# Performance work log

Hardware: AMD Instinct MI355X
Metric: run time of the kernel (lower is better)

## Reference

```python
import jax, jax.numpy as jnp
import numpy as np

B, L = 16, 512          # samples x tokens-per-sample
S = B * L               # total packed tokens
H, HKV, D = 16, 4, 128  # query heads, kv heads, head_dim
G = H // HKV            # GQA group size
HID = 2048
EPS = 1e-6


def rmsnorm(x, w):
    # Qwen2RMSNorm: fp32 variance, scale by weight
    v = jnp.mean(x.astype(jnp.float32) ** 2, axis=-1, keepdims=True)
    return (x.astype(jnp.float32) * jax.lax.rsqrt(v + EPS)).astype(x.dtype) * w


def rotate_half(x):
    x1, x2 = jnp.split(x, 2, axis=-1)
    return jnp.concatenate([-x2, x1], axis=-1)


def setup_inputs() -> dict:
    key = jax.random.key(0)
    ks = jax.random.split(key, 24)
    f = lambda k, shp, s=0.02: (jax.random.normal(k, shp, dtype=jnp.float32) * s)
    inp = {
        'packed_sequence_und': f(ks[0], (S // 2, HID), 1.0),
        'packed_sequence_gen': f(ks[1], (S // 2, HID), 1.0),
        # und tokens on even slots, gen on odd slots -> irregular scatter
        'packed_und_token_indexes': jnp.arange(0, S, 2, dtype=jnp.int32),
        'packed_gen_token_indexes': jnp.arange(1, S, 2, dtype=jnp.int32),
        # und-path projections (q/k/v have bias, o does not)
        'q_w': f(ks[2], (H * D, HID)), 'q_b': f(ks[3], (H * D,)),
        'k_w': f(ks[4], (HKV * D, HID)), 'k_b': f(ks[5], (HKV * D,)),
        'v_w': f(ks[6], (HKV * D, HID)), 'v_b': f(ks[7], (HKV * D,)),
        'o_w': f(ks[8], (HID, H * D)),
        # gen-path (moe_gen) projections
        'q_w_g': f(ks[9], (H * D, HID)), 'q_b_g': f(ks[10], (H * D,)),
        'k_w_g': f(ks[11], (HKV * D, HID)), 'k_b_g': f(ks[12], (HKV * D,)),
        'v_w_g': f(ks[13], (HKV * D, HID)), 'v_b_g': f(ks[14], (HKV * D,)),
        'o_w_g': f(ks[15], (HID, H * D)),
        # qk-norm weights
        'qn_w': jnp.ones((D,), jnp.float32), 'kn_w': jnp.ones((D,), jnp.float32),
        'qn_w_g': jnp.ones((D,), jnp.float32), 'kn_w_g': jnp.ones((D,), jnp.float32),
    }
    # RoPE cos/sin for packed positions (position resets per sample)
    pos = jnp.tile(jnp.arange(L, dtype=jnp.float32), B)            # [S]
    inv_freq = 1.0 / (1e6 ** (jnp.arange(0, D, 2, dtype=jnp.float32) / D))
    freqs = pos[:, None] * inv_freq[None, :]                       # [S, D/2]
    emb = jnp.concatenate([freqs, freqs], axis=-1)                 # [S, D]
    inp['packed_cos'] = jnp.cos(emb)
    inp['packed_sin'] = jnp.sin(emb)
    return inp


def reference(packed_sequence_und, packed_sequence_gen, packed_cos, packed_sin,
              packed_und_token_indexes, packed_gen_token_indexes,
              q_w, q_b, k_w, k_b, v_w, v_b, o_w,
              q_w_g, q_b_g, k_w_g, k_b_g, v_w_g, v_b_g, o_w_g,
              qn_w, kn_w, qn_w_g, kn_w_g):
    ui, gi = packed_und_token_indexes, packed_gen_token_indexes
    # dual-path QKV projection + index scatter into shared packed buffers
    q = jnp.zeros((S, H * D), jnp.float32)
    q = q.at[ui].set(packed_sequence_und @ q_w.T + q_b)
    q = q.at[gi].set(packed_sequence_gen @ q_w_g.T + q_b_g)
    k = jnp.zeros((S, HKV * D), jnp.float32)
    k = k.at[ui].set(packed_sequence_und @ k_w.T + k_b)
    k = k.at[gi].set(packed_sequence_gen @ k_w_g.T + k_b_g)
    v = jnp.zeros((S, HKV * D), jnp.float32)
    v = v.at[ui].set(packed_sequence_und @ v_w.T + v_b)
    v = v.at[gi].set(packed_sequence_gen @ v_w_g.T + v_b_g)

    q = q.reshape(S, H, D)
    k = k.reshape(S, HKV, D)
    v = v.reshape(S, HKV, D)

    # per-stream QK RMSNorm, scattered back
    q = jnp.zeros_like(q).at[ui].set(rmsnorm(q[ui], qn_w)).at[gi].set(rmsnorm(q[gi], qn_w_g))
    k = jnp.zeros_like(k).at[ui].set(rmsnorm(k[ui], kn_w)).at[gi].set(rmsnorm(k[gi], kn_w_g))

    # RoPE (unsqueeze_dim=1)
    cos, sin = packed_cos[:, None, :], packed_sin[:, None, :]
    q = q * cos + rotate_half(q) * sin
    k = k * cos + rotate_half(k) * sin

    # block-diagonal causal attention over packed samples (GQA)
    qb_ = q.reshape(B, L, HKV, G, D)
    kb_ = k.reshape(B, L, HKV, D)
    vb_ = v.reshape(B, L, HKV, D)
    scale = 1.0 / np.sqrt(D)
    scores = jnp.einsum('bqhgd,bkhd->bhgqk', qb_, kb_) * scale   # [B,HKV,G,L,L]
    causal = jnp.tril(jnp.ones((L, L), bool))
    scores = jnp.where(causal, scores, -jnp.inf)
    probs = jax.nn.softmax(scores, axis=-1)
    out = jnp.einsum('bhgqk,bkhd->bqhgd', probs, vb_)            # [B,L,HKV,G,D]
    out = out.reshape(S, H * D)

    out_und = out[ui] @ o_w.T
    out_gen = out[gi] @ o_w_g.T
    return (out_und, out_gen)
```

## Files before the change

### kernel.cpp

```cpp
#include <hip/hip_runtime.h>

typedef __bf16 bf16;
typedef __bf16 bf16x8 __attribute__((ext_vector_type(8)));
typedef float  f32x4  __attribute__((ext_vector_type(4)));

#define HALF   4096
#define S_TOT  8192
#define HID    2048
#define NH     16
#define NKV    4
#define DH     128
#define LSEQ   512

typedef const __attribute__((address_space(1))) void* as1_cvp;
typedef __attribute__((address_space(3))) void* as3_vp;

__device__ __forceinline__ void gl2lds16(const void* g, void* l) {
    __builtin_amdgcn_global_load_lds((as1_cvp)g, (as3_vp)l, 16, 0, 0);
}

#define VMCNT(n) asm volatile("s_waitcnt vmcnt(" #n ")" ::: "memory")

struct CvtArgs {
    const float* src[10];
    bf16*        dst[10];
    int          n4[10];
};
__global__ __launch_bounds__(256) void k_convert_multi(CvtArgs a, int total4) {
    int i = blockIdx.x * 256 + threadIdx.x;
    if (i >= total4) return;
    int off = i;
    #pragma unroll
    for (int s = 0; s < 10; ++s) {
        if (off < a.n4[s]) {
            float4 v = ((const float4*)a.src[s])[off];
            union { bf16 b[4]; ushort4 u; } t;
            t.b[0] = (bf16)v.x; t.b[1] = (bf16)v.y; t.b[2] = (bf16)v.z; t.b[3] = (bf16)v.w;
            ((ushort4*)a.dst[s])[off] = t.u;
            return;
        }
        off -= a.n4[s];
    }
}

__global__ void k_invtyp(const int* __restrict__ ui, const int* __restrict__ gi,
                         int* __restrict__ it) {
    int t = blockIdx.x * 256 + threadIdx.x;
    if (t < HALF) { it[ui[t]] = t << 1; it[gi[t]] = (t << 1) | 1; }
}

#define C0 0
#define C1 16384
#define C2 32768
#define C3 49152

#define STG2(MB, KC, DST)                                                       \
    gl2lds16((MB) + (KC) + go0, (DST) + wave*1024);                             \
    gl2lds16((MB) + (KC) + go1, (DST) + 8192 + wave*1024);

#define PH(RD, MH, DOB, STG, TAIL)                                              \
  {                                                                             \
    _Pragma("unroll")                                                           \
    for (int im = 0; im < 4; ++im)                                              \
        a_[im] = *(const bf16x8*)(sAb + (RD) + (MH)*4096 + im*1024 + abase);    \
    if (DOB) {                                                                  \
        _Pragma("unroll")                                                       \
        for (int jn = 0; jn < 4; ++jn)                                          \
            b_[jn] = *(const bf16x8*)(sBb + (RD) + jn*1024 + bbase);            \
    }                                                                           \
    STG;                                                                        \
    __builtin_amdgcn_s_barrier();                                               \
    __builtin_amdgcn_s_setprio(1);                                              \
    _Pragma("unroll")                                                           \
    for (int im = 0; im < 4; ++im)                                              \
      _Pragma("unroll")                                                         \
      for (int jn = 0; jn < 4; ++jn)                                            \
        acc[(MH)*4+im][jn] = __builtin_amdgcn_mfma_f32_16x16x32_bf16(           \
            a_[im], b_[jn], acc[(MH)*4+im][jn], 0, 0, 0);                       \
    __builtin_amdgcn_s_setprio(0);                                              \
    TAIL;                                                                       \
    __builtin_amdgcn_s_barrier();                                               \
  }

__device__ __forceinline__ void gemm256_core(
    const bf16* __restrict__ A, const bf16* __restrict__ B,
    int m0, int n0, int tid, char* sAb, char* sBb, f32x4 (&acc)[8][4])
{
    const int lane = tid & 63;
    const int lm = lane & 15, kq = lane >> 4;
    const int wave = tid >> 6;
    const int wm = wave >> 2, wn = wave & 3;

    const int swz16 = (kq ^ ((lm >> 1) & 3)) * 16;
    const int abase = wm*8192 + lm*64 + swz16;
    const int bbase = wn*4096 + lm*64 + swz16;

    int go0, go1;
    {
        const int s0 = tid,        r0 = s0 >> 2, c0 = (s0 & 3) ^ ((r0 >> 1) & 3);
        const int s1 = 512 + tid,  r1 = s1 >> 2, c1 = (s1 & 3) ^ ((r1 >> 1) & 3);
        go0 = r0*HID + c0*8;
        go1 = r1*HID + c1*8;
    }
    const bf16* Ab = A + (size_t)m0*HID;
    const bf16* Bb = B + (size_t)n0*HID;

    bf16x8 a_[4], b_[4];

    STG2(Ab, 0,  sAb + C0);  STG2(Ab, 32, sAb + C1);
    STG2(Bb, 0,  sBb + C0);  STG2(Bb, 32, sBb + C1);
    STG2(Ab, 64, sAb + C2);  STG2(Bb, 64, sBb + C2);
    VMCNT(4);
    __builtin_amdgcn_s_barrier();

    #pragma unroll 1
    for (int i = 0; i < 15; ++i) {
        const int kc = 128*i;
        PH(C0, 0, 1, STG2(Ab, kc+96,  sAb+C3), (void)0);
        PH(C0, 1, 0, STG2(Bb, kc+96,  sBb+C3), (void)0);
        PH(C1, 0, 1, STG2(Ab, kc+128, sAb+C0), (void)0);
        PH(C1, 1, 0, STG2(Bb, kc+128, sBb+C0), VMCNT(4));
        PH(C2, 0, 1, STG2(Ab, kc+160, sAb+C1), (void)0);
        PH(C2, 1, 0, STG2(Bb, kc+160, sBb+C1), (void)0);
        PH(C3, 0, 1, STG2(Ab, kc+192, sAb+C2), (void)0);
        PH(C3, 1, 0, STG2(Bb, kc+192, sBb+C2), VMCNT(4));
    }
    {
        PH(C0, 0, 1, STG2(Ab, 2016, sAb+C3), (void)0);
        PH(C0, 1, 0, STG2(Bb, 2016, sBb+C3), (void)0);
        PH(C1, 0, 1, (void)0, (void)0);
        PH(C1, 1, 0, (void)0, VMCNT(0));
        PH(C2, 0, 1, (void)0, (void)0);
        PH(C2, 1, 0, (void)0, (void)0);
        PH(C3, 0, 1, (void)0, (void)0);
        PH(C3, 1, 0, (void)0, (void)0);
    }
}

__global__ __launch_bounds__(512, 2) void k_gemm_qkv(
    const bf16* __restrict__ Xu, const bf16* __restrict__ Xg,
    const bf16* __restrict__ Wu, const bf16* __restrict__ Wg,
    const float* __restrict__ qbu, const float* __restrict__ kbu, const float* __restrict__ vbu,
    const float* __restrict__ qbg, const float* __restrict__ kbg, const float* __restrict__ vbg,
    const int* __restrict__ ui, const int* __restrict__ gi,
    bf16* __restrict__ qo, bf16* __restrict__ ko, bf16* __restrict__ vo)
{
    __shared__ __align__(16) bf16 sA[4][256*32];
    __shared__ __align__(16) bf16 sB[4][256*32];

    const int lin = blockIdx.x;
    const int idx = (lin & 7) * 48 + (lin >> 3);
    const int gen = idx / 192;
    const int rem = idx - gen * 192;
    const int my  = rem / 12;
    const int nx_ = rem - my * 12;
    const int m0 = my * 256, n0 = nx_ * 256;

    const bf16* X = gen ? Xg : Xu;
    const bf16* W = gen ? Wg : Wu;
    const float* qb = gen ? qbg : qbu;
    const float* kb = gen ? kbg : kbu;
    const float* vb = gen ? vbg : vbu;
    const int* idxmap = gen ? gi : ui;

    const int tid = threadIdx.x;
    const int wave = tid >> 6, lane = tid & 63;
    const int lm = lane & 15, kq = lane >> 4;
    const int wm = wave >> 2, wn = wave & 3;

    f32x4 acc[8][4] = {};
    gemm256_core(X, W, m0, n0, tid, (char*)&sA[0][0], (char*)&sB[0][0], acc);

    #pragma unroll
    for (int im = 0; im < 8; ++im) {
        int srow[4];
        #pragma unroll
        for (int r = 0; r < 4; ++r) srow[r] = idxmap[m0 + wm*128 + im*16 + kq*4 + r];
        #pragma unroll
        for (int jn = 0; jn < 4; ++jn) {
            const int o = n0 + wn*64 + jn*16 + lm;
            bf16* dst; float bias; int off0, ld;
            if (o < 2048)      { dst = qo; ld = 2048; off0 = o;        bias = qb[o]; }
            else if (o < 2560) { dst = ko; ld = 512;  off0 = o - 2048; bias = kb[o-2048]; }
            else               { dst = vo; ld = 512;  off0 = o - 2560; bias = vb[o-2560]; }
            #pragma unroll
            for (int r = 0; r < 4; ++r)
                dst[(size_t)srow[r]*ld + off0] = (bf16)(acc[im][jn][r] + bias);
        }
    }
}

__global__ __launch_bounds__(256) void k_norm_rope(
    bf16* __restrict__ qbuf, bf16* __restrict__ kbuf,
    const float* __restrict__ cosb, const float* __restrict__ sinb,
    const int* __restrict__ invtyp,
    const float* __restrict__ qnu, const float* __restrict__ qng,
    const float* __restrict__ knu, const float* __restrict__ kng)
{
    const int row = blockIdx.x * 4 + (threadIdx.x >> 6);
    const int lane = threadIdx.x & 63;
    const int s = row / (NH + NKV), hh = row % (NH + NKV);
    const int isg = invtyp[s] & 1;
    bf16* ptr; const float* w; float qs;
    if (hh < NH) { ptr = qbuf + (size_t)s*HID + hh*DH;           w = isg ? qng : qnu;
                   qs = 0.08838834764831845f * 1.4426950408889634f; }
    else         { ptr = kbuf + (size_t)s*(NKV*DH) + (hh-NH)*DH; w = isg ? kng : knu;
                   qs = 1.0f; }

    const unsigned u = *(const unsigned*)((const unsigned short*)ptr + 2*lane);
    const float f0 = __uint_as_float(u << 16);
    const float f1 = __uint_as_float(u & 0xffff0000u);
    float ss = f0*f0 + f1*f1;
    #pragma unroll
    for (int m = 32; m; m >>= 1) ss += __shfl_xor(ss, m, 64);
    const float r = rsqrtf(ss * (1.0f/128.0f) + 1e-6f);
    const float2 wv = *(const float2*)(w + 2*lane);
    const float xn0 = f0 * r * wv.x;
    const float xn1 = f1 * r * wv.y;
    const float po0 = __shfl_xor(xn0, 32, 64);
    const float po1 = __shfl_xor(xn1, 32, 64);
    const float2 c2 = *(const float2*)(cosb + (size_t)s*DH + 2*lane);
    const float2 s2 = *(const float2*)(sinb + (size_t)s*DH + 2*lane);
    const float sg = (lane < 32) ? -1.0f : 1.0f;
    const float o0 = (xn0 * c2.x + sg * po0 * s2.x) * qs;
    const float o1 = (xn1 * c2.y + sg * po1 * s2.y) * qs;
    union { unsigned short us[2]; unsigned u; } t;
    bf16 b0 = (bf16)o0, b1 = (bf16)o1;
    t.us[0] = *(unsigned short*)&b0; t.us[1] = *(unsigned short*)&b1;
    *(unsigned*)((unsigned short*)ptr + 2*lane) = t.u;
}

__global__ __launch_bounds__(256) void k_vtrans(const bf16* __restrict__ v, bf16* __restrict__ vt)
{
    __shared__ __align__(16) bf16 sT[64 * 132];
    const int kvh = blockIdx.y;
    const int s0 = blockIdx.x * 64;
    const int b = s0 >> 9;
    const int pos0 = s0 & 511;
    const int tid = threadIdx.x;

    #pragma unroll
    for (int i = 0; i < 4; ++i) {
        const int c = i*256 + tid;
        const int rowi = c >> 4, col8 = c & 15;
        const uint4 d = *(const uint4*)(v + (size_t)(s0 + rowi)*(NKV*DH) + kvh*DH + col8*8);
        uint2* lp = (uint2*)&sT[rowi*132 + col8*8];
        lp[0] = make_uint2(d.x, d.y);
        lp[1] = make_uint2(d.z, d.w);
    }
    __syncthreads();
    const int dd = tid >> 1, half = tid & 1;
    __align__(16) bf16 tmp[32];
    #pragma unroll
    for (int p = 0; p < 32; ++p) tmp[p] = sT[(half*32 + p)*132 + dd];
    bf16* dst = vt + ((size_t)(b*NKV + kvh)*DH + dd)*LSEQ + pos0 + half*32;
    #pragma unroll
    for (int q = 0; q < 8; ++q) ((ushort4*)dst)[q] = ((ushort4*)tmp)[q];
}

__global__ __launch_bounds__(256) void k_attn(
    const bf16* __restrict__ qbuf, const bf16* __restrict__ kbuf,
    const bf16* __restrict__ vt, const int* __restrict__ invtyp,
    bf16* __restrict__ aop_u, bf16* __restrict__ aop_g)
{
    __shared__ __align__(16) bf16 sK[2][64*128];
    __shared__ __align__(16) bf16 sV[2][128*64];
    __shared__ __align__(16) bf16 sP[4][16*72];

    const int qt = 7 - blockIdx.x;
    const int h = blockIdx.y, b = blockIdx.z;
    const int kvh = h >> 2;
    const int tid = threadIdx.x, wave = tid >> 6, lane = tid & 63;
    const int lm = lane & 15, kq = lane >> 4;
    const int q0 = qt * 64;

    bf16x8 qfrag[4];
    {
        const bf16* qp = qbuf + ((size_t)(b*LSEQ + q0 + wave*16 + lm))*HID + h*DH;
        #pragma unroll
        for (int ks = 0; ks < 4; ++ks)
            qfrag[ks] = *(const bf16x8*)(qp + ks*32 + kq*8);
    }

    const bf16* kbase = kbuf + ((size_t)(b*LSEQ))*(NKV*DH) + kvh*DH;
    const bf16* vbase = vt + ((size_t)(b*NKV + kvh)*DH)*LSEQ;

    f32x4 accO[8] = {};
    float lpart[4] = {0.f, 0.f, 0.f, 0.f};
    bf16* const sPw = &sP[wave][0];

    {
        const bf16* kp = kbase;
        const bf16* vp = vbase;
        #pragma unroll
        for (int i = 0; i < 4; ++i) {
            const int g = i*4 + wave;
            const int ch = g*64 + lane;
            { const int row = ch >> 4, cp = ch & 15;
              const int c = (cp & 8) | ((cp ^ row) & 7);
              gl2lds16(kp + (size_t)row*(NKV*DH) + c*8, (char*)&sK[0][0] + (size_t)g*1024); }
            { const int d = ch >> 3, cp = ch & 7;
              const int c = (cp ^ d) & 7;
              gl2lds16(vp + (size_t)d*LSEQ + c*8, (char*)&sV[0][0] + (size_t)g*1024); }
        }
    }

    for (int kt = 0; kt <= qt; ++kt) {
        const int cur = kt & 1;
        __syncthreads();

        if (kt < qt) {
            const bf16* kp = kbase + (size_t)((kt+1)*64)*(NKV*DH);
            const bf16* vp = vbase + (kt+1)*64;
            const int nxt = cur ^ 1;
            #pragma unroll
            for (int i = 0; i < 4; ++i) {
                const int g = i*4 + wave;
                const int ch = g*64 + lane;
                { const int row = ch >> 4, cp = ch & 15;
                  const int c = (cp & 8) | ((cp ^ row) & 7);
                  gl2lds16(kp + (size_t)row*(NKV*DH) + c*8, (char*)&sK[nxt][0] + (size_t)g*1024); }
                { const int d = ch >> 3, cp = ch & 7;
                  const int c = (cp ^ d) & 7;
                  gl2lds16(vp + (size_t)d*LSEQ + c*8, (char*)&sV[nxt][0] + (size_t)g*1024); }
            }
        }

        f32x4 s4[4] = {};
        #pragma unroll
        for (int ks = 0; ks < 4; ++ks) {
            const int cq = ks*4 + kq;
            const int cs = (cq & 8) | ((cq ^ lm) & 7);
            #pragma unroll
            for (int nt = 0; nt < 4; ++nt) {
                bf16x8 bk = *(const bf16x8*)&sK[cur][(nt*16 + lm)*128 + cs*8];
                s4[nt] = __builtin_amdgcn_mfma_f32_16x16x32_bf16(qfrag[ks], bk, s4[nt], 0, 0, 0);
            }
        }

        const bool diag = (kt == qt);
        #pragma unroll
        for (int r = 0; r < 4; ++r) {
            const int rloc = wave*16 + kq*4 + r;
            float v0 = s4[0][r], v1 = s4[1][r], v2 = s4[2][r], v3 = s4[3][r];
            if (diag) {
                if (lm      > rloc) v0 = -1e30f;
                if (lm + 16 > rloc) v1 = -1e30f;
                if (lm + 32 > rloc) v2 = -1e30f;
                if (lm + 48 > rloc) v3 = -1e30f;
            }
            const float p0 = exp2f(v0);
            const float p1 = exp2f(v1);
            const float p2 = exp2f(v2);
            const float p3 = exp2f(v3);
            lpart[r] += (p0 + p1) + (p2 + p3);
            const int prow = (kq*4 + r) * 72;
            sPw[prow + lm]      = (bf16)p0;
            sPw[prow + 16 + lm] = (bf16)p1;
            sPw[prow + 32 + lm] = (bf16)p2;
            sPw[prow + 48 + lm] = (bf16)p3;
        }

        #pragma unroll
        for (int pc = 0; pc < 2; ++pc) {
            bf16x8 ap = *(const bf16x8*)&sPw[lm*72 + pc*32 + kq*8];
            #pragma unroll
            for (int dt = 0; dt < 8; ++dt) {
                const int cv = (pc*4 + kq);
                const int cs = (cv ^ lm) & 7;
                bf16x8 bv = *(const bf16x8*)&sV[cur][(dt*16 + lm)*64 + cs*8];
                accO[dt] = __builtin_amdgcn_mfma_f32_16x16x32_bf16(ap, bv, accO[dt], 0, 0, 0);
            }
        }
    }

    #pragma unroll
    for (int r = 0; r < 4; ++r) {
        float l = lpart[r];
        l += __shfl_xor(l, 1, 64);
        l += __shfl_xor(l, 2, 64);
        l += __shfl_xor(l, 4, 64);
        l += __shfl_xor(l, 8, 64);
        const int srow = b*LSEQ + q0 + wave*16 + kq*4 + r;
        const int code = invtyp[srow];
        bf16* dst = (code & 1) ? aop_g : aop_u;
        const size_t off = (size_t)(code >> 1)*HID + h*DH;
        const float inv_l = 1.0f / l;
        #pragma unroll
        for (int dt = 0; dt < 8; ++dt)
            dst[off + dt*16 + lm] = (bf16)(accO[dt][r] * inv_l);
    }
}

__global__ __launch_bounds__(512, 2) void k_gemm_out(
    const bf16* __restrict__ Au, const bf16* __restrict__ Ag,
    const bf16* __restrict__ Wu, const bf16* __restrict__ Wg,
    float* __restrict__ out)
{
    __shared__ __align__(16) bf16 sA[4][256*32];
    __shared__ __align__(16) bf16 sB[4][256*32];

    const int lin = blockIdx.x;
    const int idx = (lin & 7) * 32 + (lin >> 3);
    const int gen = idx / 128;
    const int rem = idx - gen * 128;
    const int my  = rem >> 3;
    const int nx_ = rem & 7;
    const int m0 = my * 256, n0 = nx_ * 256;

    const bf16* A = gen ? Ag : Au;
    const bf16* W = gen ? Wg : Wu;
    float* O = out + (size_t)gen * HALF * HID;

    const int tid = threadIdx.x;
    const int wave = tid >> 6, lane = tid & 63;
    const int lm = lane & 15, kq = lane >> 4;
    const int wm = wave >> 2, wn = wave & 3;

    f32x4 acc[8][4] = {};
    gemm256_core(A, W, m0, n0, tid, (char*)&sA[0][0], (char*)&sB[0][0], acc);

    #pragma unroll
    for (int im = 0; im < 8; ++im)
        #pragma unroll
        for (int jn = 0; jn < 4; ++jn)
            #pragma unroll
            for (int r = 0; r < 4; ++r)
                O[(size_t)(m0 + wm*128 + im*16 + kq*4 + r)*HID + (n0 + wn*64 + jn*16 + lm)]
                    = acc[im][jn][r];
}

extern "C" void kernel_launch(void* const* d_in, const int* in_sizes, int n_in,
                              void* d_out, int out_size, void* d_ws, size_t ws_size,
                              hipStream_t stream)
{
    (void)in_sizes; (void)n_in; (void)out_size; (void)ws_size;
    const float* x_u  = (const float*)d_in[0];
    const float* x_g  = (const float*)d_in[1];
    const int*   ui   = (const int*)d_in[2];
    const int*   gi   = (const int*)d_in[3];
    const float* q_w  = (const float*)d_in[4];
    const float* q_b  = (const float*)d_in[5];
    const float* k_w  = (const float*)d_in[6];
    const float* k_b  = (const float*)d_in[7];
    const float* v_w  = (const float*)d_in[8];
    const float* v_b  = (const float*)d_in[9];
    const float* o_w  = (const float*)d_in[10];
    const float* q_wg = (const float*)d_in[11];
    const float* q_bg = (const float*)d_in[12];
    const float* k_wg = (const float*)d_in[13];
    const float* k_bg = (const float*)d_in[14];
    const float* v_wg = (const float*)d_in[15];
    const float* v_bg = (const float*)d_in[16];
    const float* o_wg = (const float*)d_in[17];
    const float* qn_u = (const float*)d_in[18];
    const float* kn_u = (const float*)d_in[19];
    const float* qn_g = (const float*)d_in[20];
    const float* kn_g = (const float*)d_in[21];
    const float* cosb = (const float*)d_in[22];
    const float* sinb = (const float*)d_in[23];

    char* w = (char*)d_ws;
    auto alloc = [&](size_t bytes) { char* p = w; w += (bytes + 255) & ~(size_t)255; return p; };
    bf16* xb_u   = (bf16*)alloc((size_t)HALF*HID*2);
    bf16* xb_g   = (bf16*)alloc((size_t)HALF*HID*2);
    bf16* wqkv_u = (bf16*)alloc((size_t)3072*HID*2);
    bf16* wqkv_g = (bf16*)alloc((size_t)3072*HID*2);
    bf16* wo_u   = (bf16*)alloc((size_t)HID*HID*2);
    bf16* wo_g   = (bf16*)alloc((size_t)HID*HID*2);
    bf16* qbuf   = (bf16*)alloc((size_t)S_TOT*HID*2);
    bf16* kbuf   = (bf16*)alloc((size_t)S_TOT*NKV*DH*2);
    bf16* vbuf   = (bf16*)alloc((size_t)S_TOT*NKV*DH*2);
    bf16* vtb    = (bf16*)alloc((size_t)S_TOT*NKV*DH*2);
    int*  invtyp = (int*)alloc((size_t)S_TOT*4);
    bf16* aop_u = xb_u;
    bf16* aop_g = xb_g;

    CvtArgs ca;
    int total4 = 0, si = 0;
    auto seg = [&](const float* s, bf16* d, size_t n) {
        ca.src[si] = s; ca.dst[si] = d; ca.n4[si] = (int)(n / 4);
        total4 += (int)(n / 4); ++si;
    };
    seg(x_u,  xb_u,                (size_t)HALF*HID);
    seg(x_g,  xb_g,                (size_t)HALF*HID);
    seg(q_w,  wqkv_u,              (size_t)2048*HID);
    seg(k_w,  wqkv_u + 2048*HID,   (size_t)512*HID);
    seg(v_w,  wqkv_u + 2560*HID,   (size_t)512*HID);
    seg(q_wg, wqkv_g,              (size_t)2048*HID);
    seg(k_wg, wqkv_g + 2048*HID,   (size_t)512*HID);
    seg(v_wg, wqkv_g + 2560*HID,   (size_t)512*HID);
    seg(o_w,  wo_u,                (size_t)HID*HID);
    seg(o_wg, wo_g,                (size_t)HID*HID);
    k_convert_multi<<<(total4 + 255)/256, 256, 0, stream>>>(ca, total4);

    k_invtyp<<<16, 256, 0, stream>>>(ui, gi, invtyp);

    k_gemm_qkv<<<dim3(384), 512, 0, stream>>>(
        xb_u, xb_g, wqkv_u, wqkv_g,
        q_b, k_b, v_b, q_bg, k_bg, v_bg,
        ui, gi, qbuf, kbuf, vbuf);

    k_norm_rope<<<(S_TOT*(NH+NKV))/4, 256, 0, stream>>>(
        qbuf, kbuf, cosb, sinb, invtyp, qn_u, qn_g, kn_u, kn_g);

    k_vtrans<<<dim3(S_TOT/64, NKV), 256, 0, stream>>>(vbuf, vtb);

    k_attn<<<dim3(LSEQ/64, NH, 16), 256, 0, stream>>>(
        qbuf, kbuf, vtb, invtyp, aop_u, aop_g);

    k_gemm_out<<<dim3(256), 512, 0, stream>>>(
        aop_u, aop_g, wo_u, wo_g, (float*)d_out);
}
```

Measured before the change: 525.9 us.

## Pair causal attention tiles, simplify QKV GEMM, per-segment convert blocks

```diff
diff --git a/kernel.cpp b/kernel.cpp
--- a/kernel.cpp
+++ b/kernel.cpp
@@ -26,27 +26,99 @@
     bf16*        dst[10];
     int          n4[10];
 };
-__global__ __launch_bounds__(256) void k_convert_multi(CvtArgs a, int total4) {
-    int i = blockIdx.x * 256 + threadIdx.x;
-    if (i >= total4) return;
-    int off = i;
-    #pragma unroll
-    for (int s = 0; s < 10; ++s) {
-        if (off < a.n4[s]) {
-            float4 v = ((const float4*)a.src[s])[off];
-            union { bf16 b[4]; ushort4 u; } t;
-            t.b[0] = (bf16)v.x; t.b[1] = (bf16)v.y; t.b[2] = (bf16)v.z; t.b[3] = (bf16)v.w;
-            ((ushort4*)a.dst[s])[off] = t.u;
-            return;
-        }
-        off -= a.n4[s];
-    }
+__global__ __launch_bounds__(256) void k_convert_seg(CvtArgs a) {
+    int rem = blockIdx.x;
+    const float* src; bf16* dst;
+    if      (rem < 8192)           { src=a.src[0]; dst=a.dst[0]; }
+    else if ((rem -= 8192) < 8192) { src=a.src[1]; dst=a.dst[1]; }
+    else if ((rem -= 8192) < 4096) { src=a.src[2]; dst=a.dst[2]; }
+    else if ((rem -= 4096) < 1024) { src=a.src[3]; dst=a.dst[3]; }
+    else if ((rem -= 1024) < 1024) { src=a.src[4]; dst=a.dst[4]; }
+    else if ((rem -= 1024) < 4096) { src=a.src[5]; dst=a.dst[5]; }
+    else if ((rem -= 4096) < 1024) { src=a.src[6]; dst=a.dst[6]; }
+    else if ((rem -= 1024) < 1024) { src=a.src[7]; dst=a.dst[7]; }
+    else if ((rem -= 1024) < 4096) { src=a.src[8]; dst=a.dst[8]; }
+    else    { rem -= 4096;           src=a.src[9]; dst=a.dst[9]; }
+    const int i = (rem << 8) + threadIdx.x;
+    float4 v = ((const float4*)src)[i];
+    union { bf16 b[4]; ushort4 u; } t;
+    t.b[0] = (bf16)v.x; t.b[1] = (bf16)v.y; t.b[2] = (bf16)v.z; t.b[3] = (bf16)v.w;
+    ((ushort4*)dst)[i] = t.u;
 }
 
 __global__ void k_invtyp(const int* __restrict__ ui, const int* __restrict__ gi,
                          int* __restrict__ it) {
     int t = blockIdx.x * 256 + threadIdx.x;
     if (t < HALF) { it[ui[t]] = t << 1; it[gi[t]] = (t << 1) | 1; }
+}
+
+__global__ __launch_bounds__(256) void k_gemm_qkv(
+    const bf16* __restrict__ Xu, const bf16* __restrict__ Xg,
+    const bf16* __restrict__ Wu, const bf16* __restrict__ Wg,
+    const float* __restrict__ qbu, const float* __restrict__ kbu, const float* __restrict__ vbu,
+    const float* __restrict__ qbg, const float* __restrict__ kbg, const float* __restrict__ vbg,
+    const int* __restrict__ ui, const int* __restrict__ gi,
+    bf16* __restrict__ qo, bf16* __restrict__ ko, bf16* __restrict__ vo)
+{
+    const int gen = blockIdx.z;
+    const bf16* X = gen ? Xg : Xu;
+    const bf16* W = gen ? Wg : Wu;
+    const float* qb = gen ? qbg : qbu;
+    const float* kb = gen ? kbg : kbu;
+    const float* vb = gen ? vbg : vbu;
+    const int* idx = gen ? gi : ui;
+
+    __shared__ __align__(16) bf16 sA[128*32];
+    __shared__ __align__(16) bf16 sB[128*32];
+
+    const int tid = threadIdx.x;
+    const int wave = tid >> 6, lane = tid & 63;
+    const int lm = lane & 15, kq = lane >> 4;
+    const int wm = wave >> 1, wn = wave & 1;
+    const int m0 = blockIdx.y * 128, n0 = blockIdx.x * 128;
+
+    f32x4 acc[4][4] = {};
+
+    for (int k0 = 0; k0 < HID; k0 += 32) {
+        __syncthreads();
+        #pragma unroll
+        for (int i = 0; i < 2; ++i) {
+            const int g = i*4 + wave;
+            const int c = g*64 + lane;
+            const int row = c >> 2, col = c & 3;
+            gl2lds16(X + (size_t)(m0+row)*HID + k0 + col*8, (char*)sA + (size_t)g*1024);
+            gl2lds16(W + (size_t)(n0+row)*HID + k0 + col*8, (char*)sB + (size_t)g*1024);
+        }
+        __syncthreads();
+        bf16x8 a[4], b[4];
+        #pragma unroll
+        for (int i = 0; i < 4; ++i) a[i] = *(const bf16x8*)&sA[(wm*64 + i*16 + lm)*32 + kq*8];
+        #pragma unroll
+        for (int j = 0; j < 4; ++j) b[j] = *(const bf16x8*)&sB[(wn*64 + j*16 + lm)*32 + kq*8];
+        #pragma unroll
+        for (int i = 0; i < 4; ++i)
+            #pragma unroll
+            for (int j = 0; j < 4; ++j)
+                acc[i][j] = __builtin_amdgcn_mfma_f32_16x16x32_bf16(a[i], b[j], acc[i][j], 0, 0, 0);
+    }
+
+    #pragma unroll
+    for (int i = 0; i < 4; ++i) {
+        int srow[4];
+        #pragma unroll
+        for (int r = 0; r < 4; ++r) srow[r] = idx[m0 + wm*64 + i*16 + kq*4 + r];
+        #pragma unroll
+        for (int j = 0; j < 4; ++j) {
+            const int o = n0 + wn*64 + j*16 + lm;
+            bf16* dst; float bias; int off0, ld;
+            if (o < 2048)      { dst = qo; ld = 2048; off0 = o;        bias = qb[o]; }
+            else if (o < 2560) { dst = ko; ld = 512;  off0 = o - 2048; bias = kb[o-2048]; }
+            else               { dst = vo; ld = 512;  off0 = o - 2560; bias = vb[o-2560]; }
+            #pragma unroll
+            for (int r = 0; r < 4; ++r)
+                dst[(size_t)srow[r]*ld + off0] = (bf16)(acc[i][j][r] + bias);
+        }
+    }
 }
 
 #define C0 0
@@ -137,59 +209,6 @@
     }
 }
 
-__global__ __launch_bounds__(512, 2) void k_gemm_qkv(
-    const bf16* __restrict__ Xu, const bf16* __restrict__ Xg,
-    const bf16* __restrict__ Wu, const bf16* __restrict__ Wg,
-    const float* __restrict__ qbu, const float* __restrict__ kbu, const float* __restrict__ vbu,
-    const float* __restrict__ qbg, const float* __restrict__ kbg, const float* __restrict__ vbg,
-    const int* __restrict__ ui, const int* __restrict__ gi,
-    bf16* __restrict__ qo, bf16* __restrict__ ko, bf16* __restrict__ vo)
-{
-    __shared__ __align__(16) bf16 sA[4][256*32];
-    __shared__ __align__(16) bf16 sB[4][256*32];
-
-    const int lin = blockIdx.x;
-    const int idx = (lin & 7) * 48 + (lin >> 3);
-    const int gen = idx / 192;
-    const int rem = idx - gen * 192;
-    const int my  = rem / 12;
-    const int nx_ = rem - my * 12;
-    const int m0 = my * 256, n0 = nx_ * 256;
-
-    const bf16* X = gen ? Xg : Xu;
-    const bf16* W = gen ? Wg : Wu;
-    const float* qb = gen ? qbg : qbu;
-    const float* kb = gen ? kbg : kbu;
-    const float* vb = gen ? vbg : vbu;
-    const int* idxmap = gen ? gi : ui;
-
-    const int tid = threadIdx.x;
-    const int wave = tid >> 6, lane = tid & 63;
-    const int lm = lane & 15, kq = lane >> 4;
-    const int wm = wave >> 2, wn = wave & 3;
-
-    f32x4 acc[8][4] = {};
-    gemm256_core(X, W, m0, n0, tid, (char*)&sA[0][0], (char*)&sB[0][0], acc);
-
-    #pragma unroll
-    for (int im = 0; im < 8; ++im) {
-        int srow[4];
-        #pragma unroll
-        for (int r = 0; r < 4; ++r) srow[r] = idxmap[m0 + wm*128 + im*16 + kq*4 + r];
-        #pragma unroll
-        for (int jn = 0; jn < 4; ++jn) {
-            const int o = n0 + wn*64 + jn*16 + lm;
-            bf16* dst; float bias; int off0, ld;
-            if (o < 2048)      { dst = qo; ld = 2048; off0 = o;        bias = qb[o]; }
-            else if (o < 2560) { dst = ko; ld = 512;  off0 = o - 2048; bias = kb[o-2048]; }
-            else               { dst = vo; ld = 512;  off0 = o - 2560; bias = vb[o-2560]; }
-            #pragma unroll
-            for (int r = 0; r < 4; ++r)
-                dst[(size_t)srow[r]*ld + off0] = (bf16)(acc[im][jn][r] + bias);
-        }
-    }
-}
-
 __global__ __launch_bounds__(256) void k_norm_rope(
     bf16* __restrict__ qbuf, bf16* __restrict__ kbuf,
     const float* __restrict__ cosb, const float* __restrict__ sinb,
@@ -267,128 +286,135 @@
     __shared__ __align__(16) bf16 sV[2][128*64];
     __shared__ __align__(16) bf16 sP[4][16*72];
 
-    const int qt = 7 - blockIdx.x;
+    const int pr = blockIdx.x;
     const int h = blockIdx.y, b = blockIdx.z;
     const int kvh = h >> 2;
     const int tid = threadIdx.x, wave = tid >> 6, lane = tid & 63;
     const int lm = lane & 15, kq = lane >> 4;
-    const int q0 = qt * 64;
-
-    bf16x8 qfrag[4];
-    {
-        const bf16* qp = qbuf + ((size_t)(b*LSEQ + q0 + wave*16 + lm))*HID + h*DH;
-        #pragma unroll
-        for (int ks = 0; ks < 4; ++ks)
-            qfrag[ks] = *(const bf16x8*)(qp + ks*32 + kq*8);
-    }
 
     const bf16* kbase = kbuf + ((size_t)(b*LSEQ))*(NKV*DH) + kvh*DH;
     const bf16* vbase = vt + ((size_t)(b*NKV + kvh)*DH)*LSEQ;
-
-    f32x4 accO[8] = {};
-    float lpart[4] = {0.f, 0.f, 0.f, 0.f};
     bf16* const sPw = &sP[wave][0];
 
-    {
-        const bf16* kp = kbase;
-        const bf16* vp = vbase;
-        #pragma unroll
-        for (int i = 0; i < 4; ++i) {
-            const int g = i*4 + wave;
-            const int ch = g*64 + lane;
-            { const int row = ch >> 4, cp = ch & 15;
-              const int c = (cp & 8) | ((cp ^ row) & 7);
-              gl2lds16(kp + (size_t)row*(NKV*DH) + c*8, (char*)&sK[0][0] + (size_t)g*1024); }
-            { const int d = ch >> 3, cp = ch & 7;
-              const int c = (cp ^ d) & 7;
-              gl2lds16(vp + (size_t)d*LSEQ + c*8, (char*)&sV[0][0] + (size_t)g*1024); }
+    #pragma unroll 1
+    for (int t = 0; t < 2; ++t) {
+        const int qt = t ? pr : 7 - pr;
+        const int q0 = qt * 64;
+
+        bf16x8 qfrag[4];
+        {
+            const bf16* qp = qbuf + ((size_t)(b*LSEQ + q0 + wave*16 + lm))*HID + h*DH;
+            #pragma unroll
+            for (int ks = 0; ks < 4; ++ks)
+                qfrag[ks] = *(const bf16x8*)(qp + ks*32 + kq*8);
         }
-    }
-
-    for (int kt = 0; kt <= qt; ++kt) {
-        const int cur = kt & 1;
-        __syncthreads();
-
-        if (kt < qt) {
-            const bf16* kp = kbase + (size_t)((kt+1)*64)*(NKV*DH);
-            const bf16* vp = vbase + (kt+1)*64;
-            const int nxt = cur ^ 1;
+
+        f32x4 accO[8] = {};
+        float lpart[4] = {0.f, 0.f, 0.f, 0.f};
+
+        if (t) __syncthreads();
+
+        {
+            const bf16* kp = kbase;
+            const bf16* vp = vbase;
             #pragma unroll
             for (int i = 0; i < 4; ++i) {
                 const int g = i*4 + wave;
                 const int ch = g*64 + lane;
                 { const int row = ch >> 4, cp = ch & 15;
                   const int c = (cp & 8) | ((cp ^ row) & 7);
-                  gl2lds16(kp + (size_t)row*(NKV*DH) + c*8, (char*)&sK[nxt][0] + (size_t)g*1024); }
+                  gl2lds16(kp + (size_t)row*(NKV*DH) + c*8, (char*)&sK[0][0] + (size_t)g*1024); }
                 { const int d = ch >> 3, cp = ch & 7;
                   const int c = (cp ^ d) & 7;
-                  gl2lds16(vp + (size_t)d*LSEQ + c*8, (char*)&sV[nxt][0] + (size_t)g*1024); }
+                  gl2lds16(vp + (size_t)d*LSEQ + c*8, (char*)&sV[0][0] + (size_t)g*1024); }
             }
         }
 
-        f32x4 s4[4] = {};
-        #pragma unroll
-        for (int ks = 0; ks < 4; ++ks) {
-            const int cq = ks*4 + kq;
-            const int cs = (cq & 8) | ((cq ^ lm) & 7);
-            #pragma unroll
-            for (int nt = 0; nt < 4; ++nt) {
-                bf16x8 bk = *(const bf16x8*)&sK[cur][(nt*16 + lm)*128 + cs*8];
-                s4[nt] = __builtin_amdgcn_mfma_f32_16x16x32_bf16(qfrag[ks], bk, s4[nt], 0, 0, 0);
+        for (int kt = 0; kt <= qt; ++kt) {
+            const int cur = kt & 1;
+            __syncthreads();
+
+            if (kt < qt) {
+                const bf16* kp = kbase + (size_t)((kt+1)*64)*(NKV*DH);
+                const bf16* vp = vbase + (kt+1)*64;
+                const int nxt = cur ^ 1;
+                #pragma unroll
+                for (int i = 0; i < 4; ++i) {
+                    const int g = i*4 + wave;
+                    const int ch = g*64 + lane;
+                    { const int row = ch >> 4, cp = ch & 15;
+                      const int c = (cp & 8) | ((cp ^ row) & 7);
+                      gl2lds16(kp + (size_t)row*(NKV*DH) + c*8, (char*)&sK[nxt][0] + (size_t)g*1024); }
+                    { const int d = ch >> 3, cp = ch & 7;
+                      const int c = (cp ^ d) & 7;
+                      gl2lds16(vp + (size_t)d*LSEQ + c*8, (char*)&sV[nxt][0] + (size_t)g*1024); }
+                }
+            }
+
+            f32x4 s4[4] = {};
+            #pragma unroll
+            for (int ks = 0; ks < 4; ++ks) {
+                const int cq = ks*4 + kq;
+                const int cs = (cq & 8) | ((cq ^ lm) & 7);
+                #pragma unroll
+                for (int nt = 0; nt < 4; ++nt) {
+                    bf16x8 bk = *(const bf16x8*)&sK[cur][(nt*16 + lm)*128 + cs*8];
+                    s4[nt] = __builtin_amdgcn_mfma_f32_16x16x32_bf16(qfrag[ks], bk, s4[nt], 0, 0, 0);
+                }
+            }
+
+            const bool diag = (kt == qt);
+            #pragma unroll
+            for (int r = 0; r < 4; ++r) {
+                const int rloc = wave*16 + kq*4 + r;
+                float v0 = s4[0][r], v1 = s4[1][r], v2 = s4[2][r], v3 = s4[3][r];
+                if (diag) {
+                    if (lm      > rloc) v0 = -1e30f;
+                    if (lm + 16 > rloc) v1 = -1e30f;
+                    if (lm + 32 > rloc) v2 = -1e30f;
+                    if (lm + 48 > rloc) v3 = -1e30f;
+                }
+                const float p0 = exp2f(v0);
+                const float p1 = exp2f(v1);
+                const float p2 = exp2f(v2);
+                const float p3 = exp2f(v3);
+                lpart[r] += (p0 + p1) + (p2 + p3);
+                const int prow = (kq*4 + r) * 72;
+                sPw[prow + lm]      = (bf16)p0;
+                sPw[prow + 16 + lm] = (bf16)p1;
+                sPw[prow + 32 + lm] = (bf16)p2;
+                sPw[prow + 48 + lm] = (bf16)p3;
+            }
+
+            #pragma unroll
+            for (int pc = 0; pc < 2; ++pc) {
+                bf16x8 ap = *(const bf16x8*)&sPw[lm*72 + pc*32 + kq*8];
+                #pragma unroll
+                for (int dt = 0; dt < 8; ++dt) {
+                    const int cv = (pc*4 + kq);
+                    const int cs = (cv ^ lm) & 7;
+                    bf16x8 bv = *(const bf16x8*)&sV[cur][(dt*16 + lm)*64 + cs*8];
+                    accO[dt] = __builtin_amdgcn_mfma_f32_16x16x32_bf16(ap, bv, accO[dt], 0, 0, 0);
+                }
             }
         }
 
-        const bool diag = (kt == qt);
         #pragma unroll
         for (int r = 0; r < 4; ++r) {
-            const int rloc = wave*16 + kq*4 + r;
-            float v0 = s4[0][r], v1 = s4[1][r], v2 = s4[2][r], v3 = s4[3][r];
-            if (diag) {
-                if (lm      > rloc) v0 = -1e30f;
-                if (lm + 16 > rloc) v1 = -1e30f;
-                if (lm + 32 > rloc) v2 = -1e30f;
-                if (lm + 48 > rloc) v3 = -1e30f;
-            }
-            const float p0 = exp2f(v0);
-            const float p1 = exp2f(v1);
-            const float p2 = exp2f(v2);
-            const float p3 = exp2f(v3);
-            lpart[r] += (p0 + p1) + (p2 + p3);
-            const int prow = (kq*4 + r) * 72;
-            sPw[prow + lm]      = (bf16)p0;
-            sPw[prow + 16 + lm] = (bf16)p1;
-            sPw[prow + 32 + lm] = (bf16)p2;
-            sPw[prow + 48 + lm] = (bf16)p3;
+            float l = lpart[r];
+            l += __shfl_xor(l, 1, 64);
+            l += __shfl_xor(l, 2, 64);
+            l += __shfl_xor(l, 4, 64);
+            l += __shfl_xor(l, 8, 64);
+            const int srow = b*LSEQ + q0 + wave*16 + kq*4 + r;
+            const int code = invtyp[srow];
+            bf16* dst = (code & 1) ? aop_g : aop_u;
+            const size_t off = (size_t)(code >> 1)*HID + h*DH;
+            const float inv_l = 1.0f / l;
+            #pragma unroll
+            for (int dt = 0; dt < 8; ++dt)
+                dst[off + dt*16 + lm] = (bf16)(accO[dt][r] * inv_l);
         }
-
-        #pragma unroll
-        for (int pc = 0; pc < 2; ++pc) {
-            bf16x8 ap = *(const bf16x8*)&sPw[lm*72 + pc*32 + kq*8];
-            #pragma unroll
-            for (int dt = 0; dt < 8; ++dt) {
-                const int cv = (pc*4 + kq);
-                const int cs = (cv ^ lm) & 7;
-                bf16x8 bv = *(const bf16x8*)&sV[cur][(dt*16 + lm)*64 + cs*8];
-                accO[dt] = __builtin_amdgcn_mfma_f32_16x16x32_bf16(ap, bv, accO[dt], 0, 0, 0);
-            }
-        }
-    }
-
-    #pragma unroll
-    for (int r = 0; r < 4; ++r) {
-        float l = lpart[r];
-        l += __shfl_xor(l, 1, 64);
-        l += __shfl_xor(l, 2, 64);
-        l += __shfl_xor(l, 4, 64);
-        l += __shfl_xor(l, 8, 64);
-        const int srow = b*LSEQ + q0 + wave*16 + kq*4 + r;
-        const int code = invtyp[srow];
-        bf16* dst = (code & 1) ? aop_g : aop_u;
-        const size_t off = (size_t)(code >> 1)*HID + h*DH;
-        const float inv_l = 1.0f / l;
-        #pragma unroll
-        for (int dt = 0; dt < 8; ++dt)
-            dst[off + dt*16 + lm] = (bf16)(accO[dt][r] * inv_l);
     }
 }
 
@@ -477,10 +503,9 @@
     bf16* aop_g = xb_g;
 
     CvtArgs ca;
-    int total4 = 0, si = 0;
+    int si = 0;
     auto seg = [&](const float* s, bf16* d, size_t n) {
-        ca.src[si] = s; ca.dst[si] = d; ca.n4[si] = (int)(n / 4);
-        total4 += (int)(n / 4); ++si;
+        ca.src[si] = s; ca.dst[si] = d; ca.n4[si] = (int)(n / 4); ++si;
     };
     seg(x_u,  xb_u,                (size_t)HALF*HID);
     seg(x_g,  xb_g,                (size_t)HALF*HID);
@@ -492,11 +517,11 @@
     seg(v_wg, wqkv_g + 2560*HID,   (size_t)512*HID);
     seg(o_w,  wo_u,                (size_t)HID*HID);
     seg(o_wg, wo_g,                (size_t)HID*HID);
-    k_convert_multi<<<(total4 + 255)/256, 256, 0, stream>>>(ca, total4);
+    k_convert_seg<<<36864, 256, 0, stream>>>(ca);
 
     k_invtyp<<<16, 256, 0, stream>>>(ui, gi, invtyp);
 
-    k_gemm_qkv<<<dim3(384), 512, 0, stream>>>(
+    k_gemm_qkv<<<dim3(24, 32, 2), 256, 0, stream>>>(
         xb_u, xb_g, wqkv_u, wqkv_g,
         q_b, k_b, v_b, q_bg, k_bg, v_bg,
         ui, gi, qbuf, kbuf, vbuf);
@@ -506,7 +531,7 @@
 
     k_vtrans<<<dim3(S_TOT/64, NKV), 256, 0, stream>>>(vbuf, vtb);
 
-    k_attn<<<dim3(LSEQ/64, NH, 16), 256, 0, stream>>>(
+    k_attn<<<dim3(4, NH, 16), 256, 0, stream>>>(
         qbuf, kbuf, vtb, invtyp, aop_u, aop_g);
 
     k_gemm_out<<<dim3(256), 512, 0, stream>>>(
```

Measured after the change: 504.9 us. 4.0% less time.
